# Kernel tuning notes

Hardware: AMD Instinct MI355X
Metric: run time of the kernel (lower is better)

## Reference

```python
import jax, jax.numpy as jnp
import numpy as np

B, T, D, H = 16, 4096, 1024, 32
EPS = 1e-6


def setup_inputs() -> dict:
    key = jax.random.key(0)
    ks = jax.random.split(key, 12)
    inp = {
        'Z_real': jax.random.normal(ks[0], (B, T, D), jnp.float32),
        'Z_imag': jax.random.normal(ks[1], (B, T, D), jnp.float32),
        'mask': jnp.ones((B, T), jnp.float32),
        # psi_mag: Linear(1,H) -> GELU -> Linear(H,1)  (xavier gain 0.1, zero bias)
        'W1m': jax.random.normal(ks[2], (H, 1), jnp.float32) * 0.1,
        'b1m': jnp.zeros((H,), jnp.float32),
        'W2m': jax.random.normal(ks[3], (1, H), jnp.float32) * 0.1,
        'b2m': jnp.zeros((1,), jnp.float32),
        # psi_phase: Linear(2,H) -> GELU -> Linear(H,2)
        'W1p': jax.random.normal(ks[4], (H, 2), jnp.float32) * 0.1,
        'b1p': jnp.zeros((H,), jnp.float32),
        'W2p': jax.random.normal(ks[5], (2, H), jnp.float32) * 0.1,
        'b2p': jnp.zeros((2,), jnp.float32),
        'mag_scale': jnp.float32(0.1),
    }
    return inp


def reference(Z_real, Z_imag, mask, W1m, b1m, W2m, b2m, W1p, b1p, W2p, b2p, mag_scale):
    m = mask[:, :, None]  # (B,T,1)
    count = jnp.clip(jnp.sum(m, axis=1, keepdims=True), 1.0)  # (B,1,1)
    Ar = jnp.sum(Z_real * m, axis=1, keepdims=True) / count   # (B,1,D)
    Ai = jnp.sum(Z_imag * m, axis=1, keepdims=True) / count
    mag = jnp.sqrt(Ar * Ar + Ai * Ai)
    log_mag = jnp.log(mag + EPS)                               # (B,1,D)
    phase_vec = jnp.stack([Ar, Ai], axis=-1) / (mag[..., None] + EPS)  # (B,1,D,2)
    # psi_mag on scalar feature
    h = jax.nn.gelu(log_mag[..., None] @ W1m.T + b1m, approximate=False)  # (B,1,D,H)
    mag_delta = (h @ W2m.T + b2m)[..., 0]                      # (B,1,D)
    log_mag_out = log_mag + mag_scale * mag_delta
    # psi_phase on 2-vector
    hp = jax.nn.gelu(phase_vec @ W1p.T + b1p, approximate=False)  # (B,1,D,H)
    pv = hp @ W2p.T + b2p                                      # (B,1,D,2)
    norm = jnp.maximum(jnp.sqrt(jnp.sum(pv * pv, axis=-1, keepdims=True)), 1e-12)
    pv = pv / norm
    r_out = jnp.exp(log_mag_out)
    A_new_r = r_out * pv[..., 0]
    A_new_i = r_out * pv[..., 1]
    out = jnp.stack([Z_real + A_new_r, Z_imag + A_new_i], axis=0)  # (2,B,T,D)
    return out
```

## Files before the change

### kernel.cpp

```cpp
#include <hip/hip_runtime.h>
#include <math.h>

#define BB 16
#define TT 4096
#define DD 1024
#define HH 32

static constexpr float kEPS = 1e-6f;

typedef float f32x4 __attribute__((ext_vector_type(4)));

#define TCHUNK 64
__global__ __launch_bounds__(256) void reduce_kernel(
    const float* __restrict__ zr, const float* __restrict__ zi,
    const float* __restrict__ mask,
    float* __restrict__ arW, float* __restrict__ aiW, float* __restrict__ cntW) {
  const int b = blockIdx.y;
  const int t0 = blockIdx.x * TCHUNK;
  const int tid = threadIdx.x;
  const int d4 = tid * 4;

  f32x4 accR = (f32x4)(0.f);
  f32x4 accI = (f32x4)(0.f);
  float msum = 0.f;

  const size_t base = ((size_t)b * TT + t0) * DD + d4;
  const float* zrp = zr + base;
  const float* zip = zi + base;
  const float* mp = mask + (size_t)b * TT + t0;

  #pragma unroll 4
  for (int t = 0; t < TCHUNK; ++t) {
    const float m = mp[t];
    msum += m;
    f32x4 r = *(const f32x4*)(zrp + (size_t)t * DD);
    f32x4 im = *(const f32x4*)(zip + (size_t)t * DD);
    accR += r * m;
    accI += im * m;
  }

  const int o = b * DD + d4;
  atomicAdd(&arW[o + 0], accR.x);
  atomicAdd(&arW[o + 1], accR.y);
  atomicAdd(&arW[o + 2], accR.z);
  atomicAdd(&arW[o + 3], accR.w);
  atomicAdd(&aiW[o + 0], accI.x);
  atomicAdd(&aiW[o + 1], accI.y);
  atomicAdd(&aiW[o + 2], accI.z);
  atomicAdd(&aiW[o + 3], accI.w);
  if (tid == 0) atomicAdd(&cntW[b], msum);
}

__global__ __launch_bounds__(256) void mlp_kernel(
    const float* __restrict__ arW, const float* __restrict__ aiW,
    const float* __restrict__ cntW,
    const float* __restrict__ W1m, const float* __restrict__ b1m,
    const float* __restrict__ W2m, const float* __restrict__ b2m,
    const float* __restrict__ W1p, const float* __restrict__ b1p,
    const float* __restrict__ W2p, const float* __restrict__ b2p,
    const float* __restrict__ mag_scale,
    float* __restrict__ anR, float* __restrict__ anI) {
  const int i = blockIdx.x * blockDim.x + threadIdx.x;
  if (i >= BB * DD) return;
  const int b = i >> 10;

  const float count = fmaxf(cntW[b], 1.0f);
  const float Ar = arW[i] / count;
  const float Ai = aiW[i] / count;
  const float mag = sqrtf(Ar * Ar + Ai * Ai);
  const float log_mag = logf(mag + kEPS);
  const float inv_me = 1.0f / (mag + kEPS);
  const float pr = Ar * inv_me;
  const float pi = Ai * inv_me;

  float md = b2m[0];
  #pragma unroll
  for (int j = 0; j < HH; ++j) {
    float h = log_mag * W1m[j] + b1m[j];
    h = 0.5f * h * (1.0f + erff(h * 0.70710678118654752440f));
    md += h * W2m[j];
  }
  const float lmo = log_mag + mag_scale[0] * md;

  float pv0 = b2p[0];
  float pv1 = b2p[1];
  #pragma unroll
  for (int j = 0; j < HH; ++j) {
    float hp = pr * W1p[2 * j] + pi * W1p[2 * j + 1] + b1p[j];
    hp = 0.5f * hp * (1.0f + erff(hp * 0.70710678118654752440f));
    pv0 += hp * W2p[j];
    pv1 += hp * W2p[HH + j];
  }
  const float nrm = fmaxf(sqrtf(pv0 * pv0 + pv1 * pv1), 1e-12f);
  const float r_out = expf(lmo);
  anR[i] = r_out * pv0 / nrm;
  anI[i] = r_out * pv1 / nrm;
}

__global__ __launch_bounds__(256) void add_kernel(
    const float* __restrict__ zr, const float* __restrict__ zi,
    const float* __restrict__ anR, const float* __restrict__ anI,
    float* __restrict__ out) {
  const size_t N4 = (size_t)BB * TT * DD / 4;
  const size_t stride = (size_t)gridDim.x * blockDim.x;
  float* out0 = out;
  float* out1 = out + (size_t)BB * TT * DD;

  const int rb = gridDim.x - 1 - blockIdx.x;
  const size_t lane = (size_t)rb * blockDim.x + threadIdx.x;
  const long long nIter = (long long)((N4 + stride - 1) / stride);

  for (long long it = nIter - 1; it >= 0; --it) {
    const size_t i = (size_t)it * stride + lane;
    if (i >= N4) continue;
    const size_t e = i * 4;
    const int b = (int)(e >> 22);
    const int d = (int)(e & (DD - 1));
    const int o = b * DD + d;
    f32x4 ar4 = *(const f32x4*)(anR + o);
    f32x4 ai4 = *(const f32x4*)(anI + o);
    f32x4 r  = __builtin_nontemporal_load((const f32x4*)zr + i);
    f32x4 im = __builtin_nontemporal_load((const f32x4*)zi + i);
    r += ar4;
    im += ai4;
    __builtin_nontemporal_store(r, (f32x4*)out0 + i);
    __builtin_nontemporal_store(im, (f32x4*)out1 + i);
  }
}

extern "C" void kernel_launch(void* const* d_in, const int* in_sizes, int n_in,
                              void* d_out, int out_size, void* d_ws, size_t ws_size,
                              hipStream_t stream) {
  const float* zr = (const float*)d_in[0];
  const float* zi = (const float*)d_in[1];
  const float* mask = (const float*)d_in[2];
  const float* W1m = (const float*)d_in[3];
  const float* b1m = (const float*)d_in[4];
  const float* W2m = (const float*)d_in[5];
  const float* b2m = (const float*)d_in[6];
  const float* W1p = (const float*)d_in[7];
  const float* b1p = (const float*)d_in[8];
  const float* W2p = (const float*)d_in[9];
  const float* b2p = (const float*)d_in[10];
  const float* mag_scale = (const float*)d_in[11];

  float* ws = (float*)d_ws;
  float* arW = ws;
  float* aiW = ws + 16384;
  float* cntW = ws + 32768;
  float* anR = ws + 32800;
  float* anI = ws + 49184;

  (void)hipMemsetAsync(d_ws, 0, (32768 + 32) * sizeof(float), stream);

  dim3 g1(TT / TCHUNK, BB);
  reduce_kernel<<<g1, 256, 0, stream>>>(zr, zi, mask, arW, aiW, cntW);

  mlp_kernel<<<(BB * DD + 255) / 256, 256, 0, stream>>>(
      arW, aiW, cntW, W1m, b1m, W2m, b2m, W1p, b1p, W2p, b2p, mag_scale, anR, anI);

  add_kernel<<<2048, 256, 0, stream>>>(zr, zi, anR, anI, (float*)d_out);
}
```

Baseline: 313.3 us.

## Replace atomic reduction with per-chunk partials and chunked add kernel

The reduce kernel writes per-chunk partial sums instead of issuing float atomics, so the workspace memset is no longer needed. The MLP kernel now sums the 64 partials per element. The add kernel uses a 2D chunk grid that iterates rows in reverse within each block, replacing the grid-stride loop. This adds about 8 MB of partial traffic and may change the L2/MALL reuse order between the reduce and add passes.

```diff
diff --git a/kernel.cpp b/kernel.cpp
--- a/kernel.cpp
+++ b/kernel.cpp
@@ -5,18 +5,20 @@
 #define TT 4096
 #define DD 1024
 #define HH 32
+#define TCHUNK 64
+#define NCHUNK (TT / TCHUNK)
 
 static constexpr float kEPS = 1e-6f;
 
 typedef float f32x4 __attribute__((ext_vector_type(4)));
 
-#define TCHUNK 64
 __global__ __launch_bounds__(256) void reduce_kernel(
     const float* __restrict__ zr, const float* __restrict__ zi,
     const float* __restrict__ mask,
-    float* __restrict__ arW, float* __restrict__ aiW, float* __restrict__ cntW) {
+    float* __restrict__ partR, float* __restrict__ partI,
+    float* __restrict__ cntP) {
+  const int c = blockIdx.x;
   const int b = blockIdx.y;
-  const int t0 = blockIdx.x * TCHUNK;
   const int tid = threadIdx.x;
   const int d4 = tid * 4;
 
@@ -24,36 +26,30 @@
   f32x4 accI = (f32x4)(0.f);
   float msum = 0.f;
 
-  const size_t base = ((size_t)b * TT + t0) * DD + d4;
+  const size_t base = ((size_t)b * TT + (size_t)c * TCHUNK) * DD + d4;
   const float* zrp = zr + base;
   const float* zip = zi + base;
-  const float* mp = mask + (size_t)b * TT + t0;
+  const float* mp = mask + (size_t)b * TT + (size_t)c * TCHUNK;
 
-  #pragma unroll 4
+  #pragma unroll 8
   for (int t = 0; t < TCHUNK; ++t) {
     const float m = mp[t];
     msum += m;
-    f32x4 r = *(const f32x4*)(zrp + (size_t)t * DD);
+    f32x4 r  = *(const f32x4*)(zrp + (size_t)t * DD);
     f32x4 im = *(const f32x4*)(zip + (size_t)t * DD);
     accR += r * m;
     accI += im * m;
   }
 
-  const int o = b * DD + d4;
-  atomicAdd(&arW[o + 0], accR.x);
-  atomicAdd(&arW[o + 1], accR.y);
-  atomicAdd(&arW[o + 2], accR.z);
-  atomicAdd(&arW[o + 3], accR.w);
-  atomicAdd(&aiW[o + 0], accI.x);
-  atomicAdd(&aiW[o + 1], accI.y);
-  atomicAdd(&aiW[o + 2], accI.z);
-  atomicAdd(&aiW[o + 3], accI.w);
-  if (tid == 0) atomicAdd(&cntW[b], msum);
+  const size_t po = ((size_t)c * BB + b) * DD + d4;
+  *(f32x4*)(partR + po) = accR;
+  *(f32x4*)(partI + po) = accI;
+  if (tid == 0) cntP[c * BB + b] = msum;
 }
 
 __global__ __launch_bounds__(256) void mlp_kernel(
-    const float* __restrict__ arW, const float* __restrict__ aiW,
-    const float* __restrict__ cntW,
+    const float* __restrict__ partR, const float* __restrict__ partI,
+    const float* __restrict__ cntP,
     const float* __restrict__ W1m, const float* __restrict__ b1m,
     const float* __restrict__ W2m, const float* __restrict__ b2m,
     const float* __restrict__ W1p, const float* __restrict__ b1p,
@@ -61,12 +57,27 @@
     const float* __restrict__ mag_scale,
     float* __restrict__ anR, float* __restrict__ anI) {
   const int i = blockIdx.x * blockDim.x + threadIdx.x;
-  if (i >= BB * DD) return;
   const int b = i >> 10;
+  const int d = i & (DD - 1);
 
-  const float count = fmaxf(cntW[b], 1.0f);
-  const float Ar = arW[i] / count;
-  const float Ai = aiW[i] / count;
+  __shared__ float cntS;
+  if (threadIdx.x == 0) {
+    float s = 0.f;
+    for (int c = 0; c < NCHUNK; ++c) s += cntP[c * BB + b];
+    cntS = s;
+  }
+  __syncthreads();
+
+  float sR = 0.f, sI = 0.f;
+  for (int c = 0; c < NCHUNK; ++c) {
+    const size_t po = ((size_t)c * BB + b) * DD + d;
+    sR += partR[po];
+    sI += partI[po];
+  }
+
+  const float count = fmaxf(cntS, 1.0f);
+  const float Ar = sR / count;
+  const float Ai = sI / count;
   const float mag = sqrtf(Ar * Ar + Ai * Ai);
   const float log_mag = logf(mag + kEPS);
   const float inv_me = 1.0f / (mag + kEPS);
@@ -101,30 +112,30 @@
     const float* __restrict__ zr, const float* __restrict__ zi,
     const float* __restrict__ anR, const float* __restrict__ anI,
     float* __restrict__ out) {
-  const size_t N4 = (size_t)BB * TT * DD / 4;
-  const size_t stride = (size_t)gridDim.x * blockDim.x;
-  float* out0 = out;
-  float* out1 = out + (size_t)BB * TT * DD;
+  const int c = blockIdx.x;
+  const int b = blockIdx.y;
+  const int tid = threadIdx.x;
+  const int d4 = tid * 4;
 
-  const int rb = gridDim.x - 1 - blockIdx.x;
-  const size_t lane = (size_t)rb * blockDim.x + threadIdx.x;
-  const long long nIter = (long long)((N4 + stride - 1) / stride);
+  const int o = b * DD + d4;
+  const f32x4 ar4 = *(const f32x4*)(anR + o);
+  const f32x4 ai4 = *(const f32x4*)(anI + o);
 
-  for (long long it = nIter - 1; it >= 0; --it) {
-    const size_t i = (size_t)it * stride + lane;
-    if (i >= N4) continue;
-    const size_t e = i * 4;
-    const int b = (int)(e >> 22);
-    const int d = (int)(e & (DD - 1));
-    const int o = b * DD + d;
-    f32x4 ar4 = *(const f32x4*)(anR + o);
-    f32x4 ai4 = *(const f32x4*)(anI + o);
-    f32x4 r  = __builtin_nontemporal_load((const f32x4*)zr + i);
-    f32x4 im = __builtin_nontemporal_load((const f32x4*)zi + i);
+  const size_t base = ((size_t)b * TT + (size_t)c * TCHUNK) * DD + d4;
+  const float* zrp = zr + base;
+  const float* zip = zi + base;
+  float* out0 = out + base;
+  float* out1 = out + (size_t)BB * TT * DD + base;
+
+  #pragma unroll 8
+  for (int t = TCHUNK - 1; t >= 0; --t) {
+    const size_t ro = (size_t)t * DD;
+    f32x4 r  = __builtin_nontemporal_load((const f32x4*)(zrp + ro));
+    f32x4 im = __builtin_nontemporal_load((const f32x4*)(zip + ro));
     r += ar4;
     im += ai4;
-    __builtin_nontemporal_store(r, (f32x4*)out0 + i);
-    __builtin_nontemporal_store(im, (f32x4*)out1 + i);
+    __builtin_nontemporal_store(r, (f32x4*)(out0 + ro));
+    __builtin_nontemporal_store(im, (f32x4*)(out1 + ro));
   }
 }
 
@@ -145,19 +156,17 @@
   const float* mag_scale = (const float*)d_in[11];
 
   float* ws = (float*)d_ws;
-  float* arW = ws;
-  float* aiW = ws + 16384;
-  float* cntW = ws + 32768;
-  float* anR = ws + 32800;
-  float* anI = ws + 49184;
+  float* partR = ws;
+  float* partI = ws + 1048576;
+  float* cntP  = ws + 2097152;
+  float* anR   = ws + 2098176;
+  float* anI   = ws + 2114560;
 
-  (void)hipMemsetAsync(d_ws, 0, (32768 + 32) * sizeof(float), stream);
+  dim3 g(NCHUNK, BB);
+  reduce_kernel<<<g, 256, 0, stream>>>(zr, zi, mask, partR, partI, cntP);
 
-  dim3 g1(TT / TCHUNK, BB);
-  reduce_kernel<<<g1, 256, 0, stream>>>(zr, zi, mask, arW, aiW, cntW);
+  mlp_kernel<<<BB * DD / 256, 256, 0, stream>>>(
+      partR, partI, cntP, W1m, b1m, W2m, b2m, W1p, b1p, W2p, b2p, mag_scale, anR, anI);
 
-  mlp_kernel<<<(BB * DD + 255) / 256, 256, 0, stream>>>(
-      arW, aiW, cntW, W1m, b1m, W2m, b2m, W1p, b1p, W2p, b2p, mag_scale, anR, anI);
-
-  add_kernel<<<2048, 256, 0, stream>>>(zr, zi, anR, anI, (float*)d_out);
+  add_kernel<<<g, 256, 0, stream>>>(zr, zi, anR, anI, (float*)d_out);
 }
```

New measurement: 282.7 us. 1.11x faster.
